# Performance work log

Measured on AMD Instinct MI355X. Metric: run time of the kernel, lower is better.

The kernel has to match this reference:

```python
import jax, jax.numpy as jnp
import numpy as np

NUM_EMBED = 204
HEAD_DIM = 64
B, T = 4, 4096


def setup_inputs() -> dict:
    key = jax.random.key(0)
    kx, kq, kk, kv = jax.random.split(key, 4)
    x = jax.random.normal(kx, (B, T, NUM_EMBED), dtype=jnp.float32)
    s = 1.0 / np.sqrt(NUM_EMBED)
    Wq = jax.random.normal(kq, (NUM_EMBED, HEAD_DIM), dtype=jnp.float32) * s
    Wk = jax.random.normal(kk, (NUM_EMBED, HEAD_DIM), dtype=jnp.float32) * s
    Wv = jax.random.normal(kv, (NUM_EMBED, HEAD_DIM), dtype=jnp.float32) * s
    return {"x": x, "Wq": Wq, "Wk": Wk, "Wv": Wv, "mask": True}


def reference(x, Wq, Wk, Wv, mask):
    # Single-head causal attention. d_k = x.shape[-1] (as in the source, which
    # scales by sqrt of the INPUT embed dim, not head_dim).
    Bn, Tn, d_k = x.shape
    q = x @ Wq  # [B,T,H]
    k = x @ Wk  # [B,T,H]
    v = x @ Wv  # [B,T,H]
    scale = 1.0 / jnp.sqrt(jnp.asarray(d_k, dtype=x.dtype))
    scores = jnp.einsum("bqh,bkh->bqk", q, k) * scale  # [B,T,T]
    if mask:
        causal = jnp.tril(jnp.ones((Tn, Tn), dtype=bool))  # allow j <= i
        scores = jnp.where(causal, scores, jnp.finfo(scores.dtype).min)
    attn = jax.nn.softmax(scores, axis=-1)
    out = jnp.einsum("bqk,bkh->bqh", attn, v)  # [B,T,H]
    # dropout is identity in eval mode
    return out
```

## Files before the change

kernel.cpp:

```cpp
#include <hip/hip_runtime.h>

#define TSEQ   4096
#define NB     4
#define EMB    204
#define HD     64
#define WK     224
#define XSTR   232
#define KSTR   72
#define VSTR   136
#define PSTR   68
#define BIG_NEG (-3.0e38f)

typedef __attribute__((ext_vector_type(8))) short bf16x8;
typedef __attribute__((ext_vector_type(4))) float f32x4;

__device__ __forceinline__ short f2bf(float f) {
    unsigned u = __float_as_uint(f);
    return (short)((u + 0x7fffu + ((u >> 16) & 1u)) >> 16);
}
__device__ __forceinline__ float bf2f(short h) {
    return __uint_as_float(((unsigned)(unsigned short)h) << 16);
}

__global__ __launch_bounds__(256) void prep_zero_kernel(
    const float* __restrict__ Wq,
    const float* __restrict__ Wk,
    const float* __restrict__ Wv,
    short* __restrict__ Wt,
    float* __restrict__ zacc)
{
    int f = blockIdx.x * 256 + threadIdx.x;
    if (f < 3 * HD * WK) {
        int e   = f % WK;
        int h   = (f / WK) % HD;
        int mat = f / (WK * HD);
        const float* W = (mat == 0) ? Wq : (mat == 1) ? Wk : Wv;
        float v = (e < EMB) ? W[e * HD + h] : 0.f;
        Wt[f] = f2bf(v);
    }
    for (int c = blockIdx.x * 256 + threadIdx.x; c < 266240; c += 256 * 256)
        *(float4*)(zacc + c * 4) = make_float4(0.f, 0.f, 0.f, 0.f);
}

__global__ __launch_bounds__(192) void qkv_mfma_kernel(
    const float* __restrict__ x,
    const short* __restrict__ Wt,
    short* __restrict__ qg,
    short* __restrict__ kg,
    short* __restrict__ vtg)
{
    __shared__ __align__(16) short xs[16 * XSTR];

    const int t    = threadIdx.x;
    const int lane = t & 63;
    const int w    = t >> 6;
    const int l15  = lane & 15;
    const int quad = lane >> 4;
    const long long rowb = (long long)blockIdx.x * 16;

    for (int c = t; c < 816; c += 192) {
        int r = c / 51, c4 = c % 51;
        float4 xv = *(const float4*)(x + (rowb + r) * EMB + c4 * 4);
        unsigned p0 = (unsigned)(unsigned short)f2bf(xv.x)
                    | ((unsigned)(unsigned short)f2bf(xv.y) << 16);
        unsigned p1 = (unsigned)(unsigned short)f2bf(xv.z)
                    | ((unsigned)(unsigned short)f2bf(xv.w) << 16);
        uint2 pk; pk.x = p0; pk.y = p1;
        *(uint2*)(&xs[r * XSTR + c4 * 4]) = pk;
    }
    for (int c = t; c < 16 * 28; c += 192) {
        int r = c / 28, cc = c % 28;
        xs[r * XSTR + EMB + cc] = 0;
    }
    __syncthreads();

    f32x4 acc[4];
#pragma unroll
    for (int nt = 0; nt < 4; ++nt) acc[nt] = (f32x4){0.f, 0.f, 0.f, 0.f};

    const short* Wb = Wt + (size_t)w * HD * WK;
#pragma unroll
    for (int ks = 0; ks < 7; ++ks) {
        bf16x8 af = *(const bf16x8*)(&xs[l15 * XSTR + ks * 32 + quad * 8]);
#pragma unroll
        for (int nt = 0; nt < 4; ++nt) {
            bf16x8 bfr = *(const bf16x8*)(Wb + (size_t)(nt * 16 + l15) * WK
                                          + ks * 32 + quad * 8);
            acc[nt] = __builtin_amdgcn_mfma_f32_16x16x32_bf16(af, bfr, acc[nt], 0, 0, 0);
        }
    }

    const float scale = 0.07001400420f;
    if (w == 0) {
#pragma unroll
        for (int r = 0; r < 4; ++r) {
            long long grow = rowb + quad * 4 + r;
#pragma unroll
            for (int nt = 0; nt < 4; ++nt)
                qg[grow * HD + nt * 16 + l15] = f2bf(acc[nt][r] * scale);
        }
    } else if (w == 1) {
#pragma unroll
        for (int r = 0; r < 4; ++r) {
            long long grow = rowb + quad * 4 + r;
#pragma unroll
            for (int nt = 0; nt < 4; ++nt)
                kg[grow * HD + nt * 16 + l15] = f2bf(acc[nt][r]);
        }
    } else {
#pragma unroll
        for (int r = 0; r < 4; ++r) {
            long long grow = rowb + quad * 4 + r;
            int bb = (int)(grow >> 12);
            int tt = (int)(grow & 4095);
#pragma unroll
            for (int nt = 0; nt < 4; ++nt)
                vtg[((long long)bb * HD + nt * 16 + l15) * TSEQ + tt] = f2bf(acc[nt][r]);
        }
    }
}

__global__ __launch_bounds__(256) void flash_mfma_kernel(
    const short* __restrict__ qg,
    const short* __restrict__ kg,
    const short* __restrict__ vtg,
    float* __restrict__ outacc,
    float* __restrict__ lacc)
{
    __shared__ __align__(16) short Ks[128 * KSTR];
    __shared__ __align__(16) short Vt[HD * VSTR];
    __shared__ __align__(16) short Ps[4 * 16 * PSTR];

    const int t    = threadIdx.x;
    const int lane = t & 63;
    const int w    = t >> 6;
    const int pair = w & 1;
    const int par  = w >> 1;
    const int l15  = lane & 15;
    const int quad = lane >> 4;

    const int b = blockIdx.y;
    const int p = 319 - (int)blockIdx.x;

    int a, idx, s;
    if (p < 32)       { a = p >> 2;                idx = p & 3;           s = 1; }
    else if (p < 96)  { a = 8 + ((p - 32) >> 3);   idx = (p - 32) & 7;    s = 2; }
    else if (p < 192) { a = 16 + (p - 96) / 12;    idx = (p - 96) % 12;   s = 3; }
    else              { a = 24 + ((p - 192) >> 4); idx = (p - 192) & 15;  s = 4; }
    const int qt    = 4 * a + idx / s;
    const int split = idx % s;
    const int ntiles = a + 1;
    const int chunk  = (ntiles + s - 1) / s;
    const int kt0    = split * chunk;
    const int kt1    = min(ntiles, kt0 + chunk);

    const int qbase = qt * 32;
    const long long rowb = (long long)b * TSEQ;

    bf16x8 aq[2];
#pragma unroll
    for (int ss = 0; ss < 2; ++ss)
        aq[ss] = *(const bf16x8*)(qg + (rowb + qbase + pair * 16 + l15) * HD
                                  + ss * 32 + quad * 8);

    f32x4 Oacc[4];
#pragma unroll
    for (int nt = 0; nt < 4; ++nt) Oacc[nt] = (f32x4){0.f, 0.f, 0.f, 0.f};
    float lsum[4] = {0.f, 0.f, 0.f, 0.f};

    short* pw = &Ps[w * 16 * PSTR];

    for (int kt = kt0; kt < kt1; ++kt) {
        const int k0 = kt * 128;
        const bool masked = (kt == ntiles - 1);
        __syncthreads();

#pragma unroll
        for (int i = 0; i < 4; ++i) {
            int c = t + i * 256;
            int r = c >> 3, c8 = (c & 7) * 8;
            *(int4*)(&Ks[r * KSTR + c8]) =
                *(const int4*)(kg + (rowb + k0 + r) * HD + c8);
        }
#pragma unroll
        for (int i = 0; i < 4; ++i) {
            int c = t + i * 256;
            int r = c >> 4, c8 = (c & 15) * 8;
            *(int4*)(&Vt[r * VSTR + c8]) =
                *(const int4*)(vtg + ((long long)b * HD + r) * TSEQ + k0 + c8);
        }
        __syncthreads();

        f32x4 S[4];
#pragma unroll
        for (int nt = 0; nt < 4; ++nt) S[nt] = (f32x4){0.f, 0.f, 0.f, 0.f};
#pragma unroll
        for (int ss = 0; ss < 2; ++ss) {
#pragma unroll
            for (int nt = 0; nt < 4; ++nt) {
                bf16x8 bk = *(const bf16x8*)(&Ks[(par * 64 + nt * 16 + l15) * KSTR
                                                 + ss * 32 + quad * 8]);
                S[nt] = __builtin_amdgcn_mfma_f32_16x16x32_bf16(aq[ss], bk, S[nt], 0, 0, 0);
            }
        }

        if (!masked) {
#pragma unroll
            for (int r = 0; r < 4; ++r) {
#pragma unroll
                for (int nt = 0; nt < 4; ++nt) {
                    float pv = __expf(S[nt][r]);
                    short h = f2bf(pv);
                    pw[(quad * 4 + r) * PSTR + nt * 16 + l15] = h;
                    lsum[r] += bf2f(h);
                }
            }
        } else {
#pragma unroll
            for (int r = 0; r < 4; ++r) {
                const int irow = qbase + pair * 16 + quad * 4 + r;
#pragma unroll
                for (int nt = 0; nt < 4; ++nt) {
                    int j = k0 + par * 64 + nt * 16 + l15;
                    float pv = (j <= irow) ? __expf(S[nt][r]) : 0.f;
                    short h = f2bf(pv);
                    pw[(quad * 4 + r) * PSTR + nt * 16 + l15] = h;
                    lsum[r] += bf2f(h);
                }
            }
        }

#pragma unroll
        for (int ss = 0; ss < 2; ++ss) {
            bf16x8 pa = *(const bf16x8*)(&pw[l15 * PSTR + ss * 32 + quad * 8]);
#pragma unroll
            for (int nt = 0; nt < 4; ++nt) {
                bf16x8 vb = *(const bf16x8*)(&Vt[(nt * 16 + l15) * VSTR
                                                 + par * 64 + ss * 32 + quad * 8]);
                Oacc[nt] = __builtin_amdgcn_mfma_f32_16x16x32_bf16(pa, vb, Oacc[nt], 0, 0, 0);
            }
        }
    }

#pragma unroll
    for (int r = 0; r < 4; ++r) {
#pragma unroll
        for (int off = 1; off < 16; off <<= 1)
            lsum[r] += __shfl_xor(lsum[r], off, 64);
    }

    float* oa = outacc + (rowb + qbase + pair * 16) * HD;
#pragma unroll
    for (int r = 0; r < 4; ++r) {
        int row = quad * 4 + r;
#pragma unroll
        for (int nt = 0; nt < 4; ++nt)
            atomicAdd(&oa[row * HD + nt * 16 + l15], Oacc[nt][r]);
        if (l15 == 0)
            atomicAdd(&lacc[rowb + qbase + pair * 16 + row], lsum[r]);
    }
}

__global__ __launch_bounds__(256) void finalize_kernel(
    const float* __restrict__ outacc,
    const float* __restrict__ lacc,
    float* __restrict__ out)
{
    int row = blockIdx.x * 16 + (threadIdx.x >> 4);
    int c4  = (threadIdx.x & 15) * 4;
    float inv = 1.0f / lacc[row];
    float4 v = *(const float4*)(outacc + (size_t)row * HD + c4);
    v.x *= inv; v.y *= inv; v.z *= inv; v.w *= inv;
    *(float4*)(out + (size_t)row * HD + c4) = v;
}

extern "C" void kernel_launch(void* const* d_in, const int* in_sizes, int n_in,
                              void* d_out, int out_size, void* d_ws, size_t ws_size,
                              hipStream_t stream)
{
    const float* x  = (const float*)d_in[0];
    const float* Wq = (const float*)d_in[1];
    const float* Wk = (const float*)d_in[2];
    const float* Wv = (const float*)d_in[3];

    const size_t nrows = (size_t)NB * TSEQ;
    short* qg  = (short*)d_ws;
    short* kg  = qg + nrows * HD;
    short* vtg = kg + nrows * HD;
    short* Wt  = vtg + nrows * HD;
    float* outacc = (float*)(Wt + 3 * HD * WK);
    float* lacc   = outacc + nrows * HD;
    float* outp = (float*)d_out;

    prep_zero_kernel<<<dim3(256), dim3(256), 0, stream>>>(Wq, Wk, Wv, Wt, outacc);
    qkv_mfma_kernel<<<dim3(1024), dim3(192), 0, stream>>>(x, Wt, qg, kg, vtg);
    flash_mfma_kernel<<<dim3(320, NB), dim3(256), 0, stream>>>(qg, kg, vtg, outacc, lacc);
    finalize_kernel<<<dim3(1024), dim3(256), 0, stream>>>(outacc, lacc, outp);
}
```

Measured before the change: 123.8 us.

## Fuse finalize into flash kernel with tickets, widen query tiles, drop prep kernel

```diff
diff --git a/kernel.cpp b/kernel.cpp
--- a/kernel.cpp
+++ b/kernel.cpp
@@ -4,12 +4,10 @@
 #define NB     4
 #define EMB    204
 #define HD     64
-#define WK     224
 #define XSTR   232
 #define KSTR   72
 #define VSTR   136
-#define PSTR   68
-#define BIG_NEG (-3.0e38f)
+#define PSTR   136
 
 typedef __attribute__((ext_vector_type(8))) short bf16x8;
 typedef __attribute__((ext_vector_type(4))) float f32x4;
@@ -22,29 +20,11 @@
     return __uint_as_float(((unsigned)(unsigned short)h) << 16);
 }
 
-__global__ __launch_bounds__(256) void prep_zero_kernel(
+__global__ __launch_bounds__(192) void qkv_mfma_kernel(
+    const float* __restrict__ x,
     const float* __restrict__ Wq,
     const float* __restrict__ Wk,
     const float* __restrict__ Wv,
-    short* __restrict__ Wt,
-    float* __restrict__ zacc)
-{
-    int f = blockIdx.x * 256 + threadIdx.x;
-    if (f < 3 * HD * WK) {
-        int e   = f % WK;
-        int h   = (f / WK) % HD;
-        int mat = f / (WK * HD);
-        const float* W = (mat == 0) ? Wq : (mat == 1) ? Wk : Wv;
-        float v = (e < EMB) ? W[e * HD + h] : 0.f;
-        Wt[f] = f2bf(v);
-    }
-    for (int c = blockIdx.x * 256 + threadIdx.x; c < 266240; c += 256 * 256)
-        *(float4*)(zacc + c * 4) = make_float4(0.f, 0.f, 0.f, 0.f);
-}
-
-__global__ __launch_bounds__(192) void qkv_mfma_kernel(
-    const float* __restrict__ x,
-    const short* __restrict__ Wt,
     short* __restrict__ qg,
     short* __restrict__ kg,
     short* __restrict__ vtg)
@@ -74,18 +54,26 @@
     }
     __syncthreads();
 
+    const float* W = (w == 0) ? Wq : (w == 1) ? Wk : Wv;
+
     f32x4 acc[4];
 #pragma unroll
     for (int nt = 0; nt < 4; ++nt) acc[nt] = (f32x4){0.f, 0.f, 0.f, 0.f};
 
-    const short* Wb = Wt + (size_t)w * HD * WK;
 #pragma unroll
     for (int ks = 0; ks < 7; ++ks) {
         bf16x8 af = *(const bf16x8*)(&xs[l15 * XSTR + ks * 32 + quad * 8]);
+        const int e0 = ks * 32 + quad * 8;
 #pragma unroll
         for (int nt = 0; nt < 4; ++nt) {
-            bf16x8 bfr = *(const bf16x8*)(Wb + (size_t)(nt * 16 + l15) * WK
-                                          + ks * 32 + quad * 8);
+            const int h = nt * 16 + l15;
+            bf16x8 bfr;
+#pragma unroll
+            for (int j = 0; j < 8; ++j) {
+                float v = 0.f;
+                if (e0 + j < EMB) v = W[(e0 + j) * HD + h];
+                bfr[j] = f2bf(v);
+            }
             acc[nt] = __builtin_amdgcn_mfma_f32_16x16x32_bf16(af, bfr, acc[nt], 0, 0, 0);
         }
     }
@@ -125,47 +113,46 @@
     const short* __restrict__ kg,
     const short* __restrict__ vtg,
     float* __restrict__ outacc,
-    float* __restrict__ lacc)
+    float* __restrict__ lacc,
+    int*   __restrict__ tickets,
+    float* __restrict__ out)
 {
     __shared__ __align__(16) short Ks[128 * KSTR];
     __shared__ __align__(16) short Vt[HD * VSTR];
     __shared__ __align__(16) short Ps[4 * 16 * PSTR];
+    __shared__ int flagS;
 
     const int t    = threadIdx.x;
     const int lane = t & 63;
     const int w    = t >> 6;
-    const int pair = w & 1;
-    const int par  = w >> 1;
     const int l15  = lane & 15;
     const int quad = lane >> 4;
 
     const int b = blockIdx.y;
-    const int p = 319 - (int)blockIdx.x;
-
-    int a, idx, s;
-    if (p < 32)       { a = p >> 2;                idx = p & 3;           s = 1; }
-    else if (p < 96)  { a = 8 + ((p - 32) >> 3);   idx = (p - 32) & 7;    s = 2; }
-    else if (p < 192) { a = 16 + (p - 96) / 12;    idx = (p - 96) % 12;   s = 3; }
-    else              { a = 24 + ((p - 192) >> 4); idx = (p - 192) & 15;  s = 4; }
-    const int qt    = 4 * a + idx / s;
-    const int split = idx % s;
-    const int ntiles = a + 1;
+    const int p = 159 - (int)blockIdx.x;
+
+    int qt, split, s;
+    if (p < 16)       { qt = p;                 split = 0;            s = 1; }
+    else if (p < 48)  { qt = 16 + ((p - 16) >> 1); split = (p - 16) & 1; s = 2; }
+    else if (p < 96)  { qt = 32 + (p - 48) / 3;    split = (p - 48) % 3; s = 3; }
+    else              { qt = 48 + ((p - 96) >> 2); split = (p - 96) & 3; s = 4; }
+    const int ntiles = (qt >> 1) + 1;
     const int chunk  = (ntiles + s - 1) / s;
     const int kt0    = split * chunk;
     const int kt1    = min(ntiles, kt0 + chunk);
 
-    const int qbase = qt * 32;
+    const int qbase = qt * 64;
     const long long rowb = (long long)b * TSEQ;
 
     bf16x8 aq[2];
 #pragma unroll
     for (int ss = 0; ss < 2; ++ss)
-        aq[ss] = *(const bf16x8*)(qg + (rowb + qbase + pair * 16 + l15) * HD
+        aq[ss] = *(const bf16x8*)(qg + (rowb + qbase + w * 16 + l15) * HD
                                   + ss * 32 + quad * 8);
 
-    f32x4 Oacc[4];
-#pragma unroll
-    for (int nt = 0; nt < 4; ++nt) Oacc[nt] = (f32x4){0.f, 0.f, 0.f, 0.f};
+    f32x4 O[4];
+#pragma unroll
+    for (int nt = 0; nt < 4; ++nt) O[nt] = (f32x4){0.f, 0.f, 0.f, 0.f};
     float lsum[4] = {0.f, 0.f, 0.f, 0.f};
 
     short* pw = &Ps[w * 16 * PSTR];
@@ -191,14 +178,14 @@
         }
         __syncthreads();
 
-        f32x4 S[4];
-#pragma unroll
-        for (int nt = 0; nt < 4; ++nt) S[nt] = (f32x4){0.f, 0.f, 0.f, 0.f};
+        f32x4 S[8];
+#pragma unroll
+        for (int nt = 0; nt < 8; ++nt) S[nt] = (f32x4){0.f, 0.f, 0.f, 0.f};
 #pragma unroll
         for (int ss = 0; ss < 2; ++ss) {
 #pragma unroll
-            for (int nt = 0; nt < 4; ++nt) {
-                bf16x8 bk = *(const bf16x8*)(&Ks[(par * 64 + nt * 16 + l15) * KSTR
+            for (int nt = 0; nt < 8; ++nt) {
+                bf16x8 bk = *(const bf16x8*)(&Ks[(nt * 16 + l15) * KSTR
                                                  + ss * 32 + quad * 8]);
                 S[nt] = __builtin_amdgcn_mfma_f32_16x16x32_bf16(aq[ss], bk, S[nt], 0, 0, 0);
             }
@@ -208,7 +195,7 @@
 #pragma unroll
             for (int r = 0; r < 4; ++r) {
 #pragma unroll
-                for (int nt = 0; nt < 4; ++nt) {
+                for (int nt = 0; nt < 8; ++nt) {
                     float pv = __expf(S[nt][r]);
                     short h = f2bf(pv);
                     pw[(quad * 4 + r) * PSTR + nt * 16 + l15] = h;
@@ -218,10 +205,10 @@
         } else {
 #pragma unroll
             for (int r = 0; r < 4; ++r) {
-                const int irow = qbase + pair * 16 + quad * 4 + r;
-#pragma unroll
-                for (int nt = 0; nt < 4; ++nt) {
-                    int j = k0 + par * 64 + nt * 16 + l15;
+                const int irow = qbase + w * 16 + quad * 4 + r;
+#pragma unroll
+                for (int nt = 0; nt < 8; ++nt) {
+                    int j = k0 + nt * 16 + l15;
                     float pv = (j <= irow) ? __expf(S[nt][r]) : 0.f;
                     short h = f2bf(pv);
                     pw[(quad * 4 + r) * PSTR + nt * 16 + l15] = h;
@@ -231,13 +218,13 @@
         }
 
 #pragma unroll
-        for (int ss = 0; ss < 2; ++ss) {
+        for (int ss = 0; ss < 4; ++ss) {
             bf16x8 pa = *(const bf16x8*)(&pw[l15 * PSTR + ss * 32 + quad * 8]);
 #pragma unroll
             for (int nt = 0; nt < 4; ++nt) {
                 bf16x8 vb = *(const bf16x8*)(&Vt[(nt * 16 + l15) * VSTR
-                                                 + par * 64 + ss * 32 + quad * 8]);
-                Oacc[nt] = __builtin_amdgcn_mfma_f32_16x16x32_bf16(pa, vb, Oacc[nt], 0, 0, 0);
+                                                 + ss * 32 + quad * 8]);
+                O[nt] = __builtin_amdgcn_mfma_f32_16x16x32_bf16(pa, vb, O[nt], 0, 0, 0);
             }
         }
     }
@@ -249,29 +236,46 @@
             lsum[r] += __shfl_xor(lsum[r], off, 64);
     }
 
-    float* oa = outacc + (rowb + qbase + pair * 16) * HD;
-#pragma unroll
-    for (int r = 0; r < 4; ++r) {
-        int row = quad * 4 + r;
-#pragma unroll
-        for (int nt = 0; nt < 4; ++nt)
-            atomicAdd(&oa[row * HD + nt * 16 + l15], Oacc[nt][r]);
-        if (l15 == 0)
-            atomicAdd(&lacc[rowb + qbase + pair * 16 + row], lsum[r]);
-    }
-}
-
-__global__ __launch_bounds__(256) void finalize_kernel(
-    const float* __restrict__ outacc,
-    const float* __restrict__ lacc,
-    float* __restrict__ out)
-{
-    int row = blockIdx.x * 16 + (threadIdx.x >> 4);
-    int c4  = (threadIdx.x & 15) * 4;
-    float inv = 1.0f / lacc[row];
-    float4 v = *(const float4*)(outacc + (size_t)row * HD + c4);
-    v.x *= inv; v.y *= inv; v.z *= inv; v.w *= inv;
-    *(float4*)(out + (size_t)row * HD + c4) = v;
+    if (s == 1) {
+        float* op = out + (rowb + qbase + w * 16) * HD;
+#pragma unroll
+        for (int r = 0; r < 4; ++r) {
+            int row = quad * 4 + r;
+            float inv = 1.0f / lsum[r];
+#pragma unroll
+            for (int nt = 0; nt < 4; ++nt)
+                op[row * HD + nt * 16 + l15] = O[nt][r] * inv;
+        }
+    } else {
+        float* oa = outacc + (rowb + qbase + w * 16) * HD;
+#pragma unroll
+        for (int r = 0; r < 4; ++r) {
+            int row = quad * 4 + r;
+#pragma unroll
+            for (int nt = 0; nt < 4; ++nt)
+                atomicAdd(&oa[row * HD + nt * 16 + l15], O[nt][r]);
+            if (l15 == 0)
+                atomicAdd(&lacc[rowb + qbase + w * 16 + row], lsum[r]);
+        }
+        __threadfence();
+        __syncthreads();
+        if (t == 0) {
+            int old = atomicAdd(&tickets[b * 64 + qt], 1);
+            flagS = (old == s - 1) ? 1 : 0;
+        }
+        __syncthreads();
+        if (flagS) {
+            __threadfence();
+            for (int i = 0; i < 16; ++i) {
+                long long row = rowb + qbase + w * 16 + i;
+                float lv = __hip_atomic_load(&lacc[row], __ATOMIC_RELAXED,
+                                             __HIP_MEMORY_SCOPE_AGENT);
+                float ov = __hip_atomic_load(&outacc[row * HD + lane], __ATOMIC_RELAXED,
+                                             __HIP_MEMORY_SCOPE_AGENT);
+                out[row * HD + lane] = ov / lv;
+            }
+        }
+    }
 }
 
 extern "C" void kernel_launch(void* const* d_in, const int* in_sizes, int n_in,
@@ -287,13 +291,16 @@
     short* qg  = (short*)d_ws;
     short* kg  = qg + nrows * HD;
     short* vtg = kg + nrows * HD;
-    short* Wt  = vtg + nrows * HD;
-    float* outacc = (float*)(Wt + 3 * HD * WK);
+    float* outacc = (float*)(vtg + nrows * HD);
     float* lacc   = outacc + nrows * HD;
+    int*   tickets = (int*)(lacc + nrows);
     float* outp = (float*)d_out;
 
-    prep_zero_kernel<<<dim3(256), dim3(256), 0, stream>>>(Wq, Wk, Wv, Wt, outacc);
-    qkv_mfma_kernel<<<dim3(1024), dim3(192), 0, stream>>>(x, Wt, qg, kg, vtg);
-    flash_mfma_kernel<<<dim3(320, NB), dim3(256), 0, stream>>>(qg, kg, vtg, outacc, lacc);
-    finalize_kernel<<<dim3(1024), dim3(256), 0, stream>>>(outacc, lacc, outp);
-}
+    size_t zbytes = nrows * HD * sizeof(float) + nrows * sizeof(float)
+                  + (size_t)NB * 64 * sizeof(int);
+    hipMemsetAsync(outacc, 0, zbytes, stream);
+
+    qkv_mfma_kernel<<<dim3(1024), dim3(192), 0, stream>>>(x, Wq, Wk, Wv, qg, kg, vtg);
+    flash_mfma_kernel<<<dim3(160, NB), dim3(256), 0, stream>>>(
+        qg, kg, vtg, outacc, lacc, tickets, outp);
+}
```

Measured after the change: 195.4 us. 57.9% more time.
